# Performance work log

Measured on AMD Instinct MI355X. Metric: run time of the kernel, lower is better.

## Reference

```python
import jax, jax.numpy as jnp
import numpy as np

D_MODEL = 1024
N_HEADS = 16
HEAD_DIM = 64
INNER = N_HEADS * HEAD_DIM
D_FF = 4096


def ln_novar(x, w, b):
    # mean-only 'layernorm' (no variance division), per original LayerNormNoVar
    u = jnp.mean(x, axis=-1, keepdims=True)
    return w * (x - u) + b


def setup_inputs() -> dict:
    key = jax.random.key(0)
    ks = jax.random.split(key, 12)
    s = lambda k, shape, scale: jax.random.normal(k, shape, dtype=jnp.float32) * scale
    inp = {
        "src": s(ks[0], (4, 2048, D_MODEL), 1.0),
        "pre_norm_w": jnp.ones((D_MODEL,), jnp.float32),
        "pre_norm_b": jnp.zeros((D_MODEL,), jnp.float32),
        "wq": s(ks[1], (D_MODEL, INNER), 0.02),
        "wk": s(ks[2], (D_MODEL, INNER), 0.02),
        "wv": s(ks[3], (D_MODEL, INNER), 0.02),
        "w_proj": s(ks[4], (INNER, D_MODEL), 0.02),
        "b_proj": jnp.zeros((D_MODEL,), jnp.float32),
        "norm1_w": jnp.ones((D_MODEL,), jnp.float32),
        "norm1_b": jnp.zeros((D_MODEL,), jnp.float32),
        "w1": s(ks[5], (D_MODEL, D_FF), 0.02),
        "b1": jnp.zeros((D_FF,), jnp.float32),
        "w2": s(ks[6], (D_FF, D_MODEL), 0.02),
        "b2": jnp.zeros((D_MODEL,), jnp.float32),
    }
    return inp


def reference(src, pre_norm_w, pre_norm_b, wq, wk, wv, w_proj, b_proj,
              norm1_w, norm1_b, w1, b1, w2, b2):
    B, N, _ = src.shape
    scale = HEAD_DIM ** -0.5
    x = ln_novar(src, pre_norm_w, pre_norm_b)
    q = (x @ wq).reshape(B, N, N_HEADS, HEAD_DIM)
    k = (x @ wk).reshape(B, N, N_HEADS, HEAD_DIM)
    v = (x @ wv).reshape(B, N, N_HEADS, HEAD_DIM)
    attn = jnp.einsum('bqhd,bkhd->bhqk', q, k) * scale
    attn = jax.nn.softmax(attn, axis=-1)
    o = jnp.einsum('bhqk,bkhd->bqhd', attn, v).reshape(B, N, INNER)
    o = o @ w_proj + b_proj
    src = src + o
    src = ln_novar(src, norm1_w, norm1_b)
    ff = jax.nn.relu(src @ w1 + b1) @ w2 + b2
    return src + ff
```

## Files before the change

kernel.cpp:

```cpp
#include <hip/hip_runtime.h>
#include <hip/hip_bf16.h>
#include <stdint.h>

typedef __hip_bfloat16 bf16;
typedef float f32x4 __attribute__((ext_vector_type(4)));
typedef float f32x16 __attribute__((ext_vector_type(16)));
typedef short v8s __attribute__((ext_vector_type(8)));
typedef __bf16 v8bf __attribute__((ext_vector_type(8)));
typedef unsigned int v4u __attribute__((ext_vector_type(4)));
typedef unsigned int u32;

static constexpr int MROWS = 8192;
static constexpr int DM    = 1024;
static constexpr int DFF   = 4096;
static constexpr int SEQ   = 2048;

__device__ __forceinline__ f32x4 mfma16(v8s a, v8s b, f32x4 c) {
  return __builtin_amdgcn_mfma_f32_16x16x32_bf16(
      __builtin_bit_cast(v8bf, a), __builtin_bit_cast(v8bf, b), c, 0, 0, 0);
}
__device__ __forceinline__ f32x16 mfma32(v8s a, v8s b, f32x16 c) {
  return __builtin_amdgcn_mfma_f32_32x32x16_bf16(
      __builtin_bit_cast(v8bf, a), __builtin_bit_cast(v8bf, b), c, 0, 0, 0);
}

__device__ __forceinline__ void gload_lds16(const void* g, void* l) {
  __builtin_amdgcn_global_load_lds(
      (const __attribute__((address_space(1))) void*)g,
      (__attribute__((address_space(3))) void*)l, 16, 0, 0);
}

__device__ __forceinline__ u32 cvtpk_bf16(float a, float b) {
  u32 r;
  asm("v_cvt_pk_bf16_f32 %0, %1, %2" : "=v"(r) : "v"(a), "v"(b));
  return r;
}
__device__ __forceinline__ void pl32swap(u32& x, u32& y) {
  asm volatile("v_permlane32_swap_b32 %0, %1" : "+v"(x), "+v"(y));
}
__device__ __forceinline__ float fast_exp2(float x) {
  float r;
  asm("v_exp_f32 %0, %1" : "=v"(r) : "v"(x));
  return r;
}

__global__ __launch_bounds__(256) void transpose_cast(
    const float* __restrict__ W, bf16* __restrict__ WT, int K, int N) {
  __shared__ float tile[32][33];
  const int c0 = blockIdx.x * 32;
  const int r0 = blockIdx.y * 32;
  const int tx = threadIdx.x & 31, ty = threadIdx.x >> 5;
  #pragma unroll
  for (int i = 0; i < 32; i += 8)
    tile[ty + i][tx] = W[(size_t)(r0 + ty + i) * N + c0 + tx];
  __syncthreads();
  #pragma unroll
  for (int i = 0; i < 32; i += 8)
    WT[(size_t)(c0 + ty + i) * K + r0 + tx] = __float2bfloat16(tile[tx][ty + i]);
}

__global__ __launch_bounds__(256) void ln_novar_kernel(
    const float* __restrict__ x, const float* __restrict__ w,
    const float* __restrict__ b, bf16* __restrict__ ob, float* __restrict__ of) {
  const int row = blockIdx.x;
  const int t = threadIdx.x;
  const float4 v = ((const float4*)(x + (size_t)row * DM))[t];
  float s = v.x + v.y + v.z + v.w;
  #pragma unroll
  for (int off = 32; off > 0; off >>= 1) s += __shfl_down(s, off, 64);
  __shared__ float wsum[4];
  if ((t & 63) == 0) wsum[t >> 6] = s;
  __syncthreads();
  const float u = (wsum[0] + wsum[1] + wsum[2] + wsum[3]) * (1.0f / DM);
  const float4 wv = ((const float4*)w)[t];
  const float4 bv = ((const float4*)b)[t];
  const float o0 = wv.x * (v.x - u) + bv.x;
  const float o1 = wv.y * (v.y - u) + bv.y;
  const float o2 = wv.z * (v.z - u) + bv.z;
  const float o3 = wv.w * (v.w - u) + bv.w;
  bf16* op = ob + (size_t)row * DM + t * 4;
  op[0] = __float2bfloat16(o0); op[1] = __float2bfloat16(o1);
  op[2] = __float2bfloat16(o2); op[3] = __float2bfloat16(o3);
  if (of) {
    float4 o4; o4.x = o0; o4.y = o1; o4.z = o2; o4.w = o3;
    ((float4*)(of + (size_t)row * DM))[t] = o4;
  }
}

template <int EPI, int TBM>
__global__ __launch_bounds__(256) void gemm_bt(
    const bf16* __restrict__ A, const bf16* __restrict__ BT,
    bf16* __restrict__ Cb, float* __restrict__ Cf,
    const float* __restrict__ bias, const float* __restrict__ res,
    int M, int Nn, int K) {
  constexpr int WN = (TBM == 128) ? 2 : 4;
  constexpr int NW = 4 / (WN / 2) / 2 * 2;
  constexpr int NFR = (TBM == 128) ? 4 : 2;
  __shared__ __align__(16) bf16 As[TBM * 64];
  __shared__ __align__(16) bf16 Bs[128 * 64];

  const int tid = threadIdx.x;
  const int lane = tid & 63;
  const int wave = tid >> 6;
  const int wr = wave / WN;
  const int wc = wave % WN;

  const int nwg = gridDim.x;
  const int nbx = Nn / 128;
  int bid = (blockIdx.x & 7) * (nwg >> 3) + (blockIdx.x >> 3);
  const int GM = 4;
  const int grp = bid / (GM * nbx);
  const int rem = bid - grp * (GM * nbx);
  const int by = grp * GM + (rem & (GM - 1));
  const int bx = rem >> 2;
  const int tM = by * TBM, tN = bx * 128;

  f32x4 acc[4][NFR] = {};
  const int nk = K / 64;

  for (int kt = 0; kt < nk; ++kt) {
    if (kt) __syncthreads();
    const int k0 = kt * 64;
    #pragma unroll
    for (int c = 0; c < TBM / 32; ++c) {
      const int slot = c * 256 + tid;
      const int row = slot >> 3, s = slot & 7;
      const int kk = ((s ^ (row & 7)) << 3);
      gload_lds16(A + (size_t)(tM + row) * K + k0 + kk, (void*)(As + slot * 8));
    }
    #pragma unroll
    for (int c = 0; c < 4; ++c) {
      const int slot = c * 256 + tid;
      const int row = slot >> 3, s = slot & 7;
      const int kk = ((s ^ (row & 7)) << 3);
      gload_lds16(BT + (size_t)(tN + row) * K + k0 + kk, (void*)(Bs + slot * 8));
    }
    __syncthreads();

    #pragma unroll
    for (int kk = 0; kk < 2; ++kk) {
      const int kslot = kk * 4 + (lane >> 4);
      v8s af[4], bfr[NFR];
      #pragma unroll
      for (int m = 0; m < 4; ++m) {
        const int row = wr * 64 + m * 16 + (lane & 15);
        af[m] = *(const v8s*)(As + (row * 8 + (kslot ^ (row & 7))) * 8);
      }
      #pragma unroll
      for (int n = 0; n < NFR; ++n) {
        const int row = wc * (128 / WN) + n * 16 + (lane & 15);
        bfr[n] = *(const v8s*)(Bs + (row * 8 + (kslot ^ (row & 7))) * 8);
      }
      __builtin_amdgcn_s_setprio(1);
      #pragma unroll
      for (int m = 0; m < 4; ++m)
        #pragma unroll
        for (int n = 0; n < NFR; ++n)
          acc[m][n] = mfma16(af[m], bfr[n], acc[m][n]);
      __builtin_amdgcn_s_setprio(0);
    }
  }

  #pragma unroll
  for (int m = 0; m < 4; ++m) {
    #pragma unroll
    for (int n = 0; n < NFR; ++n) {
      const int row0 = tM + wr * 64 + m * 16 + ((lane >> 4) << 2);
      const int col = tN + wc * (128 / WN) + n * 16 + (lane & 15);
      #pragma unroll
      for (int r = 0; r < 4; ++r) {
        const int row = row0 + r;
        float v = acc[m][n][r];
        if (EPI == 0) {
          Cb[(size_t)row * Nn + col] = __float2bfloat16(v);
        } else if (EPI == 1) {
          v += bias[col];
          v = fmaxf(v, 0.0f);
          Cb[(size_t)row * Nn + col] = __float2bfloat16(v);
        } else if (EPI == 2) {
          v += bias[col] + res[(size_t)row * Nn + col];
          Cf[(size_t)row * Nn + col] = v;
        } else {
          const int sec = tN >> 10;
          if (sec == 0) {
            Cb[(size_t)row * Nn + col] = __float2bfloat16(v);
          } else {
            const int b = row >> 11, nn2 = row & 2047;
            const int ktt = nn2 >> 6, key = nn2 & 63;
            if (sec == 1) {
              const int ck = col - 1024;
              const int h = ck >> 6, dc = (ck >> 3) & 7, e = ck & 7;
              bf16* krp = (bf16*)(void*)bias;
              krp[((size_t)((b * 16 + h) * 32 + ktt)) * 4096 + dc * 512 +
                  key * 8 + e] = __float2bfloat16(v);
            } else {
              const int cv = col - 2048;
              const int h = cv >> 6, d = cv & 63;
              const int kc = key >> 3, e2 = key & 7;
              bf16* vrp = (bf16*)(void*)res;
              vrp[((size_t)((b * 16 + h) * 32 + ktt)) * 4096 + kc * 512 +
                  d * 8 + e2] = __float2bfloat16(v);
            }
          }
        }
      }
    }
  }
}

#define PPV(i) ((i) < 16 ? s0[(i) & 15] : s1[(i) & 15])
__global__ __launch_bounds__(256, 4) void attn_kernel(
    const bf16* __restrict__ qkv, const bf16* __restrict__ krep,
    const bf16* __restrict__ vrep, bf16* __restrict__ ob) {
  const int qt = blockIdx.x & 15;
  const int bh = blockIdx.x >> 4;
  const int b = bh >> 4, h = bh & 15;
  const int tid = threadIdx.x;
  const int lane = tid & 63, wave = tid >> 6;
  const int c = lane & 31, hi = lane >> 5;
  const float CEXP = 0.180336880111120426f;

  __shared__ __align__(16) bf16 Ks[2][4096];
  __shared__ __align__(16) bf16 Vs[2][4096];

  const int qrow = qt * 128 + wave * 32 + c;
  const bf16* qp = qkv + (size_t)(b * SEQ + qrow) * 3072 + h * 64;
  v8s qf[4];
  #pragma unroll
  for (int ks = 0; ks < 4; ++ks)
    qf[ks] = *(const v8s*)(qp + ks * 16 + hi * 8);

  f32x16 o0 = {}, o1 = {};
  float mrow = -1e30f, lrow = 0.0f;

  const size_t tilebase = (size_t)(bh * 32) * 4096;
  #pragma unroll
  for (int j = 0; j < 2; ++j) {
    gload_lds16(krep + tilebase + (tid + j * 256) * 8, &Ks[0][(tid + j * 256) * 8]);
    gload_lds16(vrep + tilebase + (tid + j * 256) * 8, &Vs[0][(tid + j * 256) * 8]);
  }
  asm volatile("s_waitcnt vmcnt(0)" ::: "memory");
  __builtin_amdgcn_s_barrier();
  asm volatile("" ::: "memory");

  for (int kt = 0; kt < 32; ++kt) {
    const int cur = kt & 1;
    if (kt < 31) {
      const size_t nb = tilebase + (size_t)(kt + 1) * 4096;
      #pragma unroll
      for (int j = 0; j < 2; ++j) {
        gload_lds16(krep + nb + (tid + j * 256) * 8, &Ks[cur ^ 1][(tid + j * 256) * 8]);
        gload_lds16(vrep + nb + (tid + j * 256) * 8, &Vs[cur ^ 1][(tid + j * 256) * 8]);
      }
    }
    const bf16* KB = Ks[cur];
    const bf16* VB = Vs[cur];

    f32x16 s0 = {}, s1 = {};
    __builtin_amdgcn_s_setprio(1);
    #pragma unroll
    for (int ks = 0; ks < 4; ++ks) {
      const int ch = (2 * ks + hi) * 512;
      v8s a0 = *(const v8s*)(KB + ch + c * 8);
      v8s a1 = *(const v8s*)(KB + ch + (c + 32) * 8);
      s0 = mfma32(a0, qf[ks], s0);
      s1 = mfma32(a1, qf[ks], s1);
    }
    __builtin_amdgcn_s_setprio(0);

    float mA = -1e30f, mB = -1e30f;
    #pragma unroll
    for (int i = 0; i < 16; i += 2) {
      mA = fmaxf(fmaxf(s0[i], s0[i + 1]), mA);
      mB = fmaxf(fmaxf(s1[i], s1[i + 1]), mB);
    }
    float tmax = fmaxf(mA, mB);
    tmax = fmaxf(tmax, __shfl_xor(tmax, 32, 64));
    if (__any(tmax - mrow > 64.0f)) {
      const float mnew = fmaxf(mrow, tmax);
      const float ef = fast_exp2((mrow - mnew) * CEXP);
      mrow = mnew;
      lrow *= ef;
      #pragma unroll
      for (int r = 0; r < 16; ++r) {
        const float efq = __shfl(ef, (r & 3) + 8 * (r >> 2) + 4 * hi, 64);
        o0[r] *= efq;
        o1[r] *= efq;
      }
    }
    const float nmc = -mrow * CEXP;
    float rs0 = 0.0f, rs1 = 0.0f;
    #pragma unroll
    for (int i = 0; i < 16; ++i) {
      s0[i] = fast_exp2(fmaf(s0[i], CEXP, nmc));
      s1[i] = fast_exp2(fmaf(s1[i], CEXP, nmc));
      rs0 += s0[i];
      rs1 += s1[i];
    }
    float rs = rs0 + rs1;
    rs += __shfl_xor(rs, 32, 64);
    lrow += rs;

    v8s pa[4];
    #pragma unroll
    for (int ks = 0; ks < 4; ++ks) {
      u32 x  = cvtpk_bf16(PPV(8 * ks + 0), PPV(8 * ks + 1));
      u32 y  = cvtpk_bf16(PPV(8 * ks + 4), PPV(8 * ks + 5));
      u32 x2 = cvtpk_bf16(PPV(8 * ks + 2), PPV(8 * ks + 3));
      u32 y2 = cvtpk_bf16(PPV(8 * ks + 6), PPV(8 * ks + 7));
      pl32swap(x, y);
      pl32swap(x2, y2);
      v4u w; w.x = x; w.y = x2; w.z = y; w.w = y2;
      pa[ks] = __builtin_bit_cast(v8s, w);
    }

    __builtin_amdgcn_s_setprio(1);
    #pragma unroll
    for (int ks = 0; ks < 4; ++ks) {
      const int ch = (2 * ks + hi) * 512;
      v8s b0 = *(const v8s*)(VB + ch + c * 8);
      v8s b1 = *(const v8s*)(VB + ch + (c + 32) * 8);
      o0 = mfma32(pa[ks], b0, o0);
      o1 = mfma32(pa[ks], b1, o1);
    }
    __builtin_amdgcn_s_setprio(0);

    asm volatile("s_waitcnt vmcnt(0)" ::: "memory");
    __builtin_amdgcn_s_barrier();
    asm volatile("" ::: "memory");
  }

  const float rl = 1.0f / lrow;
  const size_t orow0 = (size_t)(b * SEQ + qt * 128 + wave * 32);
  #pragma unroll
  for (int r = 0; r < 16; ++r) {
    const int q = (r & 3) + 8 * (r >> 2) + 4 * hi;
    const float rq = __shfl(rl, q, 64);
    bf16* op = ob + (orow0 + q) * DM + h * 64;
    op[c] = __float2bfloat16(o0[r] * rq);
    op[32 + c] = __float2bfloat16(o1[r] * rq);
  }
}

extern "C" void kernel_launch(void* const* d_in, const int* in_sizes, int n_in,
                              void* d_out, int out_size, void* d_ws,
                              size_t ws_size, hipStream_t stream) {
  const float* src   = (const float*)d_in[0];
  const float* pnw   = (const float*)d_in[1];
  const float* pnb   = (const float*)d_in[2];
  const float* wq    = (const float*)d_in[3];
  const float* wk    = (const float*)d_in[4];
  const float* wv    = (const float*)d_in[5];
  const float* wproj = (const float*)d_in[6];
  const float* bproj = (const float*)d_in[7];
  const float* n1w   = (const float*)d_in[8];
  const float* n1b   = (const float*)d_in[9];
  const float* w1    = (const float*)d_in[10];
  const float* b1    = (const float*)d_in[11];
  const float* w2    = (const float*)d_in[12];
  const float* b2    = (const float*)d_in[13];
  float* out = (float*)d_out;

  char* ws = (char*)d_ws;
  size_t off = 0;
  bf16* WTqkv = (bf16*)(ws + off); off += (size_t)3072 * 1024 * 2;
  bf16* WTprj = (bf16*)(ws + off); off += (size_t)1024 * 1024 * 2;
  bf16* WT1   = (bf16*)(ws + off); off += (size_t)4096 * 1024 * 2;
  bf16* WT2   = (bf16*)(ws + off); off += (size_t)1024 * 4096 * 2;
  bf16* xb    = (bf16*)(ws + off); off += (size_t)MROWS * DM * 2;
  bf16* qkvb  = (bf16*)(ws + off); off += (size_t)MROWS * 3072 * 2;
  bf16* obuf  = (bf16*)(ws + off); off += (size_t)MROWS * DM * 2;
  float* yf   = (float*)(ws + off); off += (size_t)MROWS * DM * 4;
  bf16* h1    = (bf16*)(ws + off); off += (size_t)MROWS * DFF * 2;
  bf16* krep = h1;
  bf16* vrep = h1 + (size_t)64 * SEQ * 64;

  const dim3 blk(256);

  transpose_cast<<<dim3(32, 32), blk, 0, stream>>>(wq, WTqkv, 1024, 1024);
  transpose_cast<<<dim3(32, 32), blk, 0, stream>>>(wk, WTqkv + 1024 * 1024, 1024, 1024);
  transpose_cast<<<dim3(32, 32), blk, 0, stream>>>(wv, WTqkv + 2048 * 1024, 1024, 1024);
  transpose_cast<<<dim3(32, 32), blk, 0, stream>>>(wproj, WTprj, 1024, 1024);
  transpose_cast<<<dim3(128, 32), blk, 0, stream>>>(w1, WT1, 1024, 4096);
  transpose_cast<<<dim3(32, 128), blk, 0, stream>>>(w2, WT2, 4096, 1024);

  ln_novar_kernel<<<MROWS, blk, 0, stream>>>(src, pnw, pnb, xb, nullptr);

  gemm_bt<3, 128><<<dim3((3072 / 128) * (MROWS / 128)), blk, 0, stream>>>(
      xb, WTqkv, qkvb, nullptr, (const float*)krep, (const float*)vrep,
      MROWS, 3072, 1024);

  attn_kernel<<<dim3(16 * 64), dim3(256), 0, stream>>>(qkvb, krep, vrep, obuf);

  gemm_bt<2, 64><<<dim3((1024 / 128) * (MROWS / 64)), blk, 0, stream>>>(
      obuf, WTprj, nullptr, yf, bproj, src, MROWS, 1024, 1024);

  ln_novar_kernel<<<MROWS, blk, 0, stream>>>(yf, n1w, n1b, xb, out);

  gemm_bt<1, 128><<<dim3((4096 / 128) * (MROWS / 128)), blk, 0, stream>>>(
      xb, WT1, h1, nullptr, b1, nullptr, MROWS, 4096, 1024);

  gemm_bt<2, 64><<<dim3((1024 / 128) * (MROWS / 64)), blk, 0, stream>>>(
      h1, WT2, nullptr, out, b2, out, MROWS, 1024, 4096);
}
```

Baseline: 420.6 us.

## Software-pipeline attention QK^T, merge weight transposes, unify GEMM tile size

The attention kernel now computes the QK^T scores for the next key tile before running softmax on the current one. It triple-buffers K in LDS with finer vmcnt waits and an extra barrier before the PV step, which lowers the occupancy hint from 4 to 3. The block index is remapped so blocks of the same head run concurrently, which should improve K/V cache reuse. The six weight transpose launches are merged into one kernel. The GEMM template drops the 64-row tile variant, so the projection and FFN2 GEMMs use 128x128 tiles with half as many workgroups, which trades fewer and larger blocks against weaker wave-level parallelism on the N=1024 GEMMs.

```diff
diff --git a/kernel.cpp b/kernel.cpp
--- a/kernel.cpp
+++ b/kernel.cpp
@@ -44,11 +44,24 @@
   return r;
 }
 
-__global__ __launch_bounds__(256) void transpose_cast(
-    const float* __restrict__ W, bf16* __restrict__ WT, int K, int N) {
+__global__ __launch_bounds__(256) void transpose_all(
+    const float* __restrict__ wq, const float* __restrict__ wk,
+    const float* __restrict__ wv, const float* __restrict__ wproj,
+    const float* __restrict__ w1, const float* __restrict__ w2,
+    bf16* __restrict__ WTqkv, bf16* __restrict__ WTprj,
+    bf16* __restrict__ WT1, bf16* __restrict__ WT2) {
   __shared__ float tile[32][33];
-  const int c0 = blockIdx.x * 32;
-  const int r0 = blockIdx.y * 32;
+  int t = blockIdx.x;
+  const float* W;
+  bf16* WT;
+  int K, N, bx, by;
+  if (t < 1024)      { W = wq;    WT = WTqkv;              K = N = 1024; bx = t & 31; by = t >> 5; }
+  else if (t < 2048) { t -= 1024; W = wk;  WT = WTqkv + 1024 * 1024; K = N = 1024; bx = t & 31; by = t >> 5; }
+  else if (t < 3072) { t -= 2048; W = wv;  WT = WTqkv + 2048 * 1024; K = N = 1024; bx = t & 31; by = t >> 5; }
+  else if (t < 4096) { t -= 3072; W = wproj; WT = WTprj;   K = N = 1024; bx = t & 31; by = t >> 5; }
+  else if (t < 8192) { t -= 4096; W = w1;  WT = WT1; K = 1024; N = 4096; bx = t & 127; by = t >> 7; }
+  else               { t -= 8192; W = w2;  WT = WT2; K = 4096; N = 1024; bx = t & 31; by = t >> 5; }
+  const int c0 = bx * 32, r0 = by * 32;
   const int tx = threadIdx.x & 31, ty = threadIdx.x >> 5;
   #pragma unroll
   for (int i = 0; i < 32; i += 8)
@@ -87,23 +100,19 @@
   }
 }
 
-template <int EPI, int TBM>
+template <int EPI>
 __global__ __launch_bounds__(256) void gemm_bt(
     const bf16* __restrict__ A, const bf16* __restrict__ BT,
     bf16* __restrict__ Cb, float* __restrict__ Cf,
     const float* __restrict__ bias, const float* __restrict__ res,
     int M, int Nn, int K) {
-  constexpr int WN = (TBM == 128) ? 2 : 4;
-  constexpr int NW = 4 / (WN / 2) / 2 * 2;
-  constexpr int NFR = (TBM == 128) ? 4 : 2;
-  __shared__ __align__(16) bf16 As[TBM * 64];
+  __shared__ __align__(16) bf16 As[128 * 64];
   __shared__ __align__(16) bf16 Bs[128 * 64];
 
   const int tid = threadIdx.x;
   const int lane = tid & 63;
   const int wave = tid >> 6;
-  const int wr = wave / WN;
-  const int wc = wave % WN;
+  const int wr = wave >> 1, wc = wave & 1;
 
   const int nwg = gridDim.x;
   const int nbx = Nn / 128;
@@ -113,26 +122,20 @@
   const int rem = bid - grp * (GM * nbx);
   const int by = grp * GM + (rem & (GM - 1));
   const int bx = rem >> 2;
-  const int tM = by * TBM, tN = bx * 128;
-
-  f32x4 acc[4][NFR] = {};
+  const int tM = by * 128, tN = bx * 128;
+
+  f32x4 acc[4][4] = {};
   const int nk = K / 64;
 
   for (int kt = 0; kt < nk; ++kt) {
     if (kt) __syncthreads();
     const int k0 = kt * 64;
     #pragma unroll
-    for (int c = 0; c < TBM / 32; ++c) {
+    for (int c = 0; c < 4; ++c) {
       const int slot = c * 256 + tid;
       const int row = slot >> 3, s = slot & 7;
       const int kk = ((s ^ (row & 7)) << 3);
       gload_lds16(A + (size_t)(tM + row) * K + k0 + kk, (void*)(As + slot * 8));
-    }
-    #pragma unroll
-    for (int c = 0; c < 4; ++c) {
-      const int slot = c * 256 + tid;
-      const int row = slot >> 3, s = slot & 7;
-      const int kk = ((s ^ (row & 7)) << 3);
       gload_lds16(BT + (size_t)(tN + row) * K + k0 + kk, (void*)(Bs + slot * 8));
     }
     __syncthreads();
@@ -140,22 +143,22 @@
     #pragma unroll
     for (int kk = 0; kk < 2; ++kk) {
       const int kslot = kk * 4 + (lane >> 4);
-      v8s af[4], bfr[NFR];
+      v8s af[4], bfr[4];
       #pragma unroll
       for (int m = 0; m < 4; ++m) {
         const int row = wr * 64 + m * 16 + (lane & 15);
         af[m] = *(const v8s*)(As + (row * 8 + (kslot ^ (row & 7))) * 8);
       }
       #pragma unroll
-      for (int n = 0; n < NFR; ++n) {
-        const int row = wc * (128 / WN) + n * 16 + (lane & 15);
+      for (int n = 0; n < 4; ++n) {
+        const int row = wc * 64 + n * 16 + (lane & 15);
         bfr[n] = *(const v8s*)(Bs + (row * 8 + (kslot ^ (row & 7))) * 8);
       }
       __builtin_amdgcn_s_setprio(1);
       #pragma unroll
       for (int m = 0; m < 4; ++m)
         #pragma unroll
-        for (int n = 0; n < NFR; ++n)
+        for (int n = 0; n < 4; ++n)
           acc[m][n] = mfma16(af[m], bfr[n], acc[m][n]);
       __builtin_amdgcn_s_setprio(0);
     }
@@ -164,9 +167,9 @@
   #pragma unroll
   for (int m = 0; m < 4; ++m) {
     #pragma unroll
-    for (int n = 0; n < NFR; ++n) {
+    for (int n = 0; n < 4; ++n) {
       const int row0 = tM + wr * 64 + m * 16 + ((lane >> 4) << 2);
-      const int col = tN + wc * (128 / WN) + n * 16 + (lane & 15);
+      const int col = tN + wc * 64 + n * 16 + (lane & 15);
       #pragma unroll
       for (int r = 0; r < 4; ++r) {
         const int row = row0 + r;
@@ -208,19 +211,18 @@
   }
 }
 
-#define PPV(i) ((i) < 16 ? s0[(i) & 15] : s1[(i) & 15])
-__global__ __launch_bounds__(256, 4) void attn_kernel(
+__global__ __launch_bounds__(256, 3) void attn_kernel(
     const bf16* __restrict__ qkv, const bf16* __restrict__ krep,
     const bf16* __restrict__ vrep, bf16* __restrict__ ob) {
-  const int qt = blockIdx.x & 15;
-  const int bh = blockIdx.x >> 4;
+  const int bh = blockIdx.x & 63;
+  const int qt = blockIdx.x >> 6;
   const int b = bh >> 4, h = bh & 15;
   const int tid = threadIdx.x;
   const int lane = tid & 63, wave = tid >> 6;
   const int c = lane & 31, hi = lane >> 5;
   const float CEXP = 0.180336880111120426f;
 
-  __shared__ __align__(16) bf16 Ks[2][4096];
+  __shared__ __align__(16) bf16 Ks[3][4096];
   __shared__ __align__(16) bf16 Vs[2][4096];
 
   const int qrow = qt * 128 + wave * 32 + c;
@@ -234,45 +236,64 @@
   float mrow = -1e30f, lrow = 0.0f;
 
   const size_t tilebase = (size_t)(bh * 32) * 4096;
-  #pragma unroll
-  for (int j = 0; j < 2; ++j) {
-    gload_lds16(krep + tilebase + (tid + j * 256) * 8, &Ks[0][(tid + j * 256) * 8]);
-    gload_lds16(vrep + tilebase + (tid + j * 256) * 8, &Vs[0][(tid + j * 256) * 8]);
-  }
-  asm volatile("s_waitcnt vmcnt(0)" ::: "memory");
-  __builtin_amdgcn_s_barrier();
-  asm volatile("" ::: "memory");
-
-  for (int kt = 0; kt < 32; ++kt) {
-    const int cur = kt & 1;
-    if (kt < 31) {
-      const size_t nb = tilebase + (size_t)(kt + 1) * 4096;
-      #pragma unroll
-      for (int j = 0; j < 2; ++j) {
-        gload_lds16(krep + nb + (tid + j * 256) * 8, &Ks[cur ^ 1][(tid + j * 256) * 8]);
-        gload_lds16(vrep + nb + (tid + j * 256) * 8, &Vs[cur ^ 1][(tid + j * 256) * 8]);
-      }
-    }
-    const bf16* KB = Ks[cur];
-    const bf16* VB = Vs[cur];
-
-    f32x16 s0 = {}, s1 = {};
-    __builtin_amdgcn_s_setprio(1);
+
+  auto STAGE_K = [&](int t) {
+    const size_t nb = tilebase + (size_t)t * 4096;
+    bf16* dst = &Ks[t % 3][0];
+    #pragma unroll
+    for (int j = 0; j < 2; ++j)
+      gload_lds16(krep + nb + (tid + j * 256) * 8, dst + (tid + j * 256) * 8);
+  };
+  auto STAGE_V = [&](int t) {
+    const size_t nb = tilebase + (size_t)t * 4096;
+    bf16* dst = &Vs[t & 1][0];
+    #pragma unroll
+    for (int j = 0; j < 2; ++j)
+      gload_lds16(vrep + nb + (tid + j * 256) * 8, dst + (tid + j * 256) * 8);
+  };
+  auto QKT = [&](const bf16* KB, f32x16& n0, f32x16& n1) {
+    n0 = f32x16{};
+    n1 = f32x16{};
     #pragma unroll
     for (int ks = 0; ks < 4; ++ks) {
       const int ch = (2 * ks + hi) * 512;
       v8s a0 = *(const v8s*)(KB + ch + c * 8);
       v8s a1 = *(const v8s*)(KB + ch + (c + 32) * 8);
-      s0 = mfma32(a0, qf[ks], s0);
-      s1 = mfma32(a1, qf[ks], s1);
-    }
-    __builtin_amdgcn_s_setprio(0);
+      n0 = mfma32(a0, qf[ks], n0);
+      n1 = mfma32(a1, qf[ks], n1);
+    }
+  };
+
+  f32x16 sA0, sA1, sB0, sB1;
+
+  STAGE_K(0);
+  STAGE_K(1);
+  STAGE_V(0);
+  asm volatile("s_waitcnt vmcnt(4)" ::: "memory");
+  __builtin_amdgcn_s_barrier();
+  asm volatile("" ::: "memory");
+  QKT(&Ks[0][0], sA0, sA1);
+
+  auto ITER = [&](int kt, f32x16& c0, f32x16& c1, f32x16& n0, f32x16& n1) {
+    if (kt + 2 < 32) STAGE_K(kt + 2);
+    if (kt + 1 < 32) STAGE_V(kt + 1);
+    if (kt <= 29)      asm volatile("s_waitcnt vmcnt(6)" ::: "memory");
+    else if (kt == 30) asm volatile("s_waitcnt vmcnt(4)" ::: "memory");
+    else               asm volatile("s_waitcnt vmcnt(2)" ::: "memory");
+    __builtin_amdgcn_s_barrier();
+    asm volatile("" ::: "memory");
+
+    if (kt + 1 < 32) {
+      __builtin_amdgcn_s_setprio(1);
+      QKT(&Ks[(kt + 1) % 3][0], n0, n1);
+      __builtin_amdgcn_s_setprio(0);
+    }
 
     float mA = -1e30f, mB = -1e30f;
     #pragma unroll
     for (int i = 0; i < 16; i += 2) {
-      mA = fmaxf(fmaxf(s0[i], s0[i + 1]), mA);
-      mB = fmaxf(fmaxf(s1[i], s1[i + 1]), mB);
+      mA = fmaxf(fmaxf(c0[i], c0[i + 1]), mA);
+      mB = fmaxf(fmaxf(c1[i], c1[i + 1]), mB);
     }
     float tmax = fmaxf(mA, mB);
     tmax = fmaxf(tmax, __shfl_xor(tmax, 32, 64));
@@ -292,28 +313,36 @@
     float rs0 = 0.0f, rs1 = 0.0f;
     #pragma unroll
     for (int i = 0; i < 16; ++i) {
-      s0[i] = fast_exp2(fmaf(s0[i], CEXP, nmc));
-      s1[i] = fast_exp2(fmaf(s1[i], CEXP, nmc));
-      rs0 += s0[i];
-      rs1 += s1[i];
+      c0[i] = fast_exp2(fmaf(c0[i], CEXP, nmc));
+      c1[i] = fast_exp2(fmaf(c1[i], CEXP, nmc));
+      rs0 += c0[i];
+      rs1 += c1[i];
     }
     float rs = rs0 + rs1;
     rs += __shfl_xor(rs, 32, 64);
     lrow += rs;
 
+    auto PPVf = [&](int i) { return i < 16 ? c0[i & 15] : c1[i & 15]; };
     v8s pa[4];
     #pragma unroll
     for (int ks = 0; ks < 4; ++ks) {
-      u32 x  = cvtpk_bf16(PPV(8 * ks + 0), PPV(8 * ks + 1));
-      u32 y  = cvtpk_bf16(PPV(8 * ks + 4), PPV(8 * ks + 5));
-      u32 x2 = cvtpk_bf16(PPV(8 * ks + 2), PPV(8 * ks + 3));
-      u32 y2 = cvtpk_bf16(PPV(8 * ks + 6), PPV(8 * ks + 7));
+      u32 x  = cvtpk_bf16(PPVf(8 * ks + 0), PPVf(8 * ks + 1));
+      u32 y  = cvtpk_bf16(PPVf(8 * ks + 4), PPVf(8 * ks + 5));
+      u32 x2 = cvtpk_bf16(PPVf(8 * ks + 2), PPVf(8 * ks + 3));
+      u32 y2 = cvtpk_bf16(PPVf(8 * ks + 6), PPVf(8 * ks + 7));
       pl32swap(x, y);
       pl32swap(x2, y2);
       v4u w; w.x = x; w.y = x2; w.z = y; w.w = y2;
       pa[ks] = __builtin_bit_cast(v8s, w);
     }
 
+    if (kt <= 29)      asm volatile("s_waitcnt vmcnt(4)" ::: "memory");
+    else if (kt == 30) asm volatile("s_waitcnt vmcnt(2)" ::: "memory");
+    else               asm volatile("s_waitcnt vmcnt(0)" ::: "memory");
+    __builtin_amdgcn_s_barrier();
+    asm volatile("" ::: "memory");
+
+    const bf16* VB = &Vs[kt & 1][0];
     __builtin_amdgcn_s_setprio(1);
     #pragma unroll
     for (int ks = 0; ks < 4; ++ks) {
@@ -324,10 +353,11 @@
       o1 = mfma32(pa[ks], b1, o1);
     }
     __builtin_amdgcn_s_setprio(0);
-
-    asm volatile("s_waitcnt vmcnt(0)" ::: "memory");
-    __builtin_amdgcn_s_barrier();
-    asm volatile("" ::: "memory");
+  };
+
+  for (int kt2 = 0; kt2 < 16; ++kt2) {
+    ITER(2 * kt2,     sA0, sA1, sB0, sB1);
+    ITER(2 * kt2 + 1, sB0, sB1, sA0, sA1);
   }
 
   const float rl = 1.0f / lrow;
@@ -377,29 +407,25 @@
 
   const dim3 blk(256);
 
-  transpose_cast<<<dim3(32, 32), blk, 0, stream>>>(wq, WTqkv, 1024, 1024);
-  transpose_cast<<<dim3(32, 32), blk, 0, stream>>>(wk, WTqkv + 1024 * 1024, 1024, 1024);
-  transpose_cast<<<dim3(32, 32), blk, 0, stream>>>(wv, WTqkv + 2048 * 1024, 1024, 1024);
-  transpose_cast<<<dim3(32, 32), blk, 0, stream>>>(wproj, WTprj, 1024, 1024);
-  transpose_cast<<<dim3(128, 32), blk, 0, stream>>>(w1, WT1, 1024, 4096);
-  transpose_cast<<<dim3(32, 128), blk, 0, stream>>>(w2, WT2, 4096, 1024);
+  transpose_all<<<dim3(12288), blk, 0, stream>>>(
+      wq, wk, wv, wproj, w1, w2, WTqkv, WTprj, WT1, WT2);
 
   ln_novar_kernel<<<MROWS, blk, 0, stream>>>(src, pnw, pnb, xb, nullptr);
 
-  gemm_bt<3, 128><<<dim3((3072 / 128) * (MROWS / 128)), blk, 0, stream>>>(
+  gemm_bt<3><<<dim3((3072 / 128) * (MROWS / 128)), blk, 0, stream>>>(
       xb, WTqkv, qkvb, nullptr, (const float*)krep, (const float*)vrep,
       MROWS, 3072, 1024);
 
   attn_kernel<<<dim3(16 * 64), dim3(256), 0, stream>>>(qkvb, krep, vrep, obuf);
 
-  gemm_bt<2, 64><<<dim3((1024 / 128) * (MROWS / 64)), blk, 0, stream>>>(
+  gemm_bt<2><<<dim3((1024 / 128) * (MROWS / 128)), blk, 0, stream>>>(
       obuf, WTprj, nullptr, yf, bproj, src, MROWS, 1024, 1024);
 
   ln_novar_kernel<<<MROWS, blk, 0, stream>>>(yf, n1w, n1b, xb, out);
 
-  gemm_bt<1, 128><<<dim3((4096 / 128) * (MROWS / 128)), blk, 0, stream>>>(
+  gemm_bt<1><<<dim3((4096 / 128) * (MROWS / 128)), blk, 0, stream>>>(
       xb, WT1, h1, nullptr, b1, nullptr, MROWS, 4096, 1024);
 
-  gemm_bt<2, 64><<<dim3((1024 / 128) * (MROWS / 64)), blk, 0, stream>>>(
+  gemm_bt<2><<<dim3((1024 / 128) * (MROWS / 128)), blk, 0, stream>>>(
       h1, WT2, nullptr, out, b2, out, MROWS, 1024, 4096);
 }
```

After: 423.5 us. About the same (+0.7%).
